# Kernel tuning notes

Measured on AMD Instinct MI355X. Metric: run time of the kernel, lower is better.

Reference implementation:

```python
import jax, jax.numpy as jnp
import numpy as np
import math

NUM_HEADS = 16
HEAD_SIZE = 64
QKT_MEAN = 0.0
QKT_STD = 0.05
APPLY_NOISE = True
NOISE_KEY = jax.random.key(42)


def quantize_activation_8bit(x):
    max_abs = jnp.maximum(jnp.max(jnp.abs(x)), 1e-08)
    scale = max_abs / 127.0
    return jnp.clip(jnp.round(x / scale), -127, 127) * scale


def quantize_weight_4bit(w):
    max_abs = jnp.maximum(jnp.max(jnp.abs(w)), 1e-08)
    scale = max_abs / 7.0
    return jnp.clip(jnp.round(w / scale), -7, 7) * scale


def setup_inputs() -> dict:
    key = jax.random.key(0)
    k1, k2, k3, k4 = jax.random.split(key, 4)
    B, S, D = 4, 1024, 1024
    hidden_states = jax.random.normal(k1, (B, S, D), dtype=jnp.float32)
    attention_mask = jnp.zeros((B, 1, 1, S), dtype=jnp.float32)
    # nn.Linear weights are [out_features, in_features]
    w_scale = 1.0 / math.sqrt(D)
    Wq = jax.random.normal(k2, (D, D), dtype=jnp.float32) * w_scale
    Wk = jax.random.normal(k3, (D, D), dtype=jnp.float32) * w_scale
    Wv = jax.random.normal(k4, (D, D), dtype=jnp.float32) * w_scale
    return {"hidden_states": hidden_states, "attention_mask": attention_mask,
            "Wq": Wq, "Wk": Wk, "Wv": Wv}


def _split_heads(x):
    B, S, _ = x.shape
    return x.reshape(B, S, NUM_HEADS, HEAD_SIZE).transpose(0, 2, 1, 3)  # [B,H,S,Dh]


def reference(hidden_states, attention_mask, Wq, Wk, Wv):
    h_q = quantize_activation_8bit(hidden_states)
    h_k = quantize_activation_8bit(hidden_states)
    Q = _split_heads(jnp.einsum('bsd,od->bso', h_q, quantize_weight_4bit(Wq)))
    K = _split_heads(jnp.einsum('bsd,od->bso', h_k, quantize_weight_4bit(Wk)))
    V = _split_heads(jnp.einsum('bsd,od->bso', hidden_states, quantize_weight_4bit(Wv)))
    qkt = jnp.einsum('bhqd,bhkd->bhqk', Q, K) / math.sqrt(HEAD_SIZE)
    if APPLY_NOISE and QKT_STD > 0:
        noise = jax.random.normal(NOISE_KEY, qkt.shape, dtype=qkt.dtype) * QKT_STD + QKT_MEAN
        qkt = qkt + noise
    qkt = qkt + attention_mask  # [B,1,1,S] broadcasts over [B,H,S,S]
    attn_weights = jax.nn.softmax(qkt, axis=-1)  # dropout is identity in eval
    ctx = jnp.einsum('bhqk,bhkd->bhqd', attn_weights, V)
    B, H, S, Dh = ctx.shape
    ctx = ctx.transpose(0, 2, 1, 3).reshape(B, S, H * Dh)
    return ctx
```

## Files before the change

kernel.cpp:

```cpp
#include <hip/hip_runtime.h>
#include <hip/hip_bf16.h>

typedef unsigned short u16;
typedef unsigned int u32;
typedef __bf16 bf16x8 __attribute__((ext_vector_type(8)));
typedef float f32x4 __attribute__((ext_vector_type(4)));

#define MFMA16(a, b, c) __builtin_amdgcn_mfma_f32_16x16x32_bf16((a), (b), (c), 0, 0, 0)

static __device__ __forceinline__ float bfbits2f(u32 b) {
    union { u32 u; float f; } c; c.u = b << 16; return c.f;
}
static __device__ __forceinline__ u32 f2bfbits(float f) {
    union { float f; u32 u; } c; c.f = f;
    return (c.u + 0x7FFFu + ((c.u >> 16) & 1u)) >> 16;
}
static __device__ __forceinline__ u32 f2bfbits_exact(float f) {
    union { float f; u32 u; } c; c.f = f;
    return c.u >> 16;
}
static __device__ __forceinline__ u32 pack_bf16x2(float lo, float hi) {
    float2 v; v.x = lo; v.y = hi;
    union { __hip_bfloat162 h; u32 u; } c;
    c.h = __float22bfloat162_rn(v);
    return c.u;
}

static __device__ __forceinline__ void noise_pu8(const u32* __restrict__ idx,
                                                 float* __restrict__ pu) {
    const u32 K1 = 42u, K2 = 0x1BD11BF0u;
    u32 x0[8], x1[8];
#pragma unroll
    for (int d = 0; d < 8; d++) { x0[d] = 0u; x1[d] = idx[d] + K1; }
#define TFR(R)                                            \
    _Pragma("unroll") for (int d = 0; d < 8; d++) {       \
        x0[d] += x1[d];                                   \
        x1[d] = __builtin_rotateleft32(x1[d], R) ^ x0[d]; \
    }
#define INJ(A, B)                                         \
    _Pragma("unroll") for (int d = 0; d < 8; d++) {       \
        x0[d] += (A); x1[d] += (B);                       \
    }
    TFR(13) TFR(15) TFR(26) TFR(6)  INJ(K1, K2 + 1u)
    TFR(17) TFR(29) TFR(16) TFR(24) INJ(K2, 2u)
    TFR(13) TFR(15) TFR(26) TFR(6)  INJ(0u, K1 + 3u)
    TFR(17) TFR(29) TFR(16) TFR(24) INJ(K1, K2 + 4u)
    TFR(13) TFR(15) TFR(26) TFR(6)  INJ(K2, 5u)
#undef TFR
#undef INJ
#pragma unroll
    for (int d = 0; d < 8; d++) {
        u32 bits = x0[d] ^ x1[d];
        float f = __uint_as_float((bits >> 9) | 0x3F800000u) - 1.0f;
        float u = fmaf(f, 2.0f, -0.99999994f);
        u = fmaxf(-0.99999994f, u);
        float t = fmaf(-u, u, 1.0f);
        float lg = __logf(t);
        float p;
        if (lg > -5.0f) {
            float z = fmaf(lg, -1.0f, -2.5f);
            p = 2.81022636e-08f;
            p = fmaf(p, z, 3.43273939e-07f);
            p = fmaf(p, z, -3.5233877e-06f);
            p = fmaf(p, z, -4.39150654e-06f);
            p = fmaf(p, z, 0.00021858087f);
            p = fmaf(p, z, -0.00125372503f);
            p = fmaf(p, z, -0.00417768164f);
            p = fmaf(p, z, 0.246640727f);
            p = fmaf(p, z, 1.50140941f);
        } else {
            float z = sqrtf(-lg) - 3.0f;
            p = -0.000200214257f;
            p = fmaf(p, z, 0.000100950558f);
            p = fmaf(p, z, 0.00134934322f);
            p = fmaf(p, z, -0.00367342844f);
            p = fmaf(p, z, 0.00573950773f);
            p = fmaf(p, z, -0.0076224613f);
            p = fmaf(p, z, 0.00943887047f);
            p = fmaf(p, z, 1.00167406f);
            p = fmaf(p, z, 2.83297682f);
        }
        pu[d] = p * u;
    }
}

__global__ __launch_bounds__(256) void absmax_k(const float* __restrict__ h,
                                                const float* __restrict__ wq,
                                                const float* __restrict__ wk,
                                                const float* __restrict__ wv,
                                                u32* __restrict__ slots) {
    int t = blockIdx.y;
    const float* src = (t == 0) ? h : (t == 1) ? wq : (t == 2) ? wk : wv;
    int n4 = ((t == 0) ? 4096 * 1024 : 1024 * 1024) / 4;
    u32 mx = 0;
    int tid = threadIdx.x;
    for (int i = blockIdx.x * blockDim.x + tid; i < n4; i += gridDim.x * blockDim.x) {
        uint4 v = ((const uint4*)src)[i];
        mx = max(mx, v.x & 0x7FFFFFFFu);
        mx = max(mx, v.y & 0x7FFFFFFFu);
        mx = max(mx, v.z & 0x7FFFFFFFu);
        mx = max(mx, v.w & 0x7FFFFFFFu);
    }
    __shared__ u32 red[256];
    red[tid] = mx;
    __syncthreads();
    for (int s = 128; s > 0; s >>= 1) {
        if (tid < s) red[tid] = max(red[tid], red[tid + s]);
        __syncthreads();
    }
    if (tid == 0) atomicMax(&slots[t], red[0]);
}

__global__ __launch_bounds__(256) void prequant_all(const float* __restrict__ hidden,
                                                    const float* __restrict__ wq,
                                                    const float* __restrict__ wk,
                                                    const float* __restrict__ wv,
                                                    u16* __restrict__ hq,
                                                    u16* __restrict__ hbf,
                                                    u16* __restrict__ wqi,
                                                    u16* __restrict__ wki,
                                                    u16* __restrict__ wvi,
                                                    const u32* __restrict__ slots) {
    int y = blockIdx.y;
    const float* src = (y == 0) ? hidden : (y == 1) ? wq : (y == 2) ? wk : wv;
    u16* dqi = (y == 0) ? hq : (y == 1) ? wqi : (y == 2) ? wki : wvi;
    u16* draw = (y == 0) ? hbf : nullptr;
    float qmax = (y == 0) ? 127.0f : 7.0f;
    int n8 = ((y == 0) ? 4096 * 1024 : 1024 * 1024) / 8;

    float amax = fmaxf(__uint_as_float(slots[y]), 1e-8f);
    float scale = amax / qmax;
    for (int i = blockIdx.x * blockDim.x + threadIdx.x; i < n8; i += gridDim.x * blockDim.x) {
        float4 a = ((const float4*)src)[2 * i];
        float4 b = ((const float4*)src)[2 * i + 1];
        float x[8] = {a.x, a.y, a.z, a.w, b.x, b.y, b.z, b.w};
        u16 qi[8], rw[8];
#pragma unroll
        for (int j = 0; j < 8; j++) {
            float q = fminf(fmaxf(rintf(x[j] / scale), -qmax), qmax);
            qi[j] = (u16)f2bfbits_exact(q);
            rw[j] = (u16)f2bfbits(x[j]);
        }
        *(uint4*)(dqi + 8 * (size_t)i) = *(const uint4*)qi;
        if (draw) *(uint4*)(draw + 8 * (size_t)i) = *(const uint4*)rw;
    }
}

__global__ __launch_bounds__(256) void qkv_gemm_all(const u16* __restrict__ hq,
                                                    const u16* __restrict__ hbf,
                                                    const u16* __restrict__ wqi,
                                                    const u16* __restrict__ wki,
                                                    const u16* __restrict__ wvi,
                                                    const u32* __restrict__ slots,
                                                    u16* __restrict__ Qb,
                                                    u16* __restrict__ Kb,
                                                    u16* __restrict__ Vtb) {
    __shared__ __align__(16) u16 As[64 * 40];
    __shared__ __align__(16) u16 Bs[64 * 40];
    int z = blockIdx.z;
    const u16* A  = (z < 2) ? hq : hbf;
    const u16* Bw = (z == 0) ? wqi : (z == 1) ? wki : wvi;
    u16* outp     = (z == 0) ? Qb : (z == 1) ? Kb : Vtb;
    int transOut = (z == 2);
    float s_a = fmaxf(__uint_as_float(slots[0]), 1e-8f) / 127.0f;
    float s_w = fmaxf(__uint_as_float(slots[z + 1]), 1e-8f) / 7.0f;
    float oscale = (z < 2) ? (s_a * s_w) : s_w;

    int tid = threadIdx.x;
    int srow = tid >> 2, scol = (tid & 3) * 8;
    int mbase = blockIdx.x * 64, nbase = blockIdx.y * 64;
    int lane = tid & 63, wv = tid >> 6;
    int quad = lane >> 4, l16 = lane & 15;

    f32x4 acc[4];
#pragma unroll
    for (int i = 0; i < 4; i++) acc[i] = (f32x4){0.f, 0.f, 0.f, 0.f};

    const u16* aptr = A + (size_t)(mbase + srow) * 1024 + scol;
    const u16* bptr = Bw + (size_t)(nbase + srow) * 1024 + scol;

    for (int k0 = 0; k0 < 1024; k0 += 32) {
        uint4 av = *(const uint4*)(aptr + k0);
        uint4 bv = *(const uint4*)(bptr + k0);
        __syncthreads();
        *(uint4*)(As + srow * 40 + scol) = av;
        *(uint4*)(Bs + srow * 40 + scol) = bv;
        __syncthreads();
        bf16x8 af = *(const bf16x8*)(As + (wv * 16 + l16) * 40 + quad * 8);
#pragma unroll
        for (int nt = 0; nt < 4; nt++) {
            bf16x8 bfr = *(const bf16x8*)(Bs + (nt * 16 + l16) * 40 + quad * 8);
            acc[nt] = MFMA16(af, bfr, acc[nt]);
        }
    }

#pragma unroll
    for (int nt = 0; nt < 4; nt++) {
#pragma unroll
        for (int r = 0; r < 4; r++) {
            float val = acc[nt][r] * oscale;
            int m = mbase + wv * 16 + quad * 4 + r;
            int o = nbase + nt * 16 + l16;
            int b = m >> 10, s = m & 1023;
            int hh = o >> 6, dh = o & 63;
            size_t off = transOut ? (((size_t)(b * 16 + hh) * 64 + dh) * 1024 + s)
                                  : (((size_t)(b * 16 + hh) * 1024 + s) * 64 + dh);
            outp[off] = (u16)f2bfbits(val);
        }
    }
}

__global__ __launch_bounds__(256, 2) void attn_kernel(const u16* __restrict__ Q,
                                                      const u16* __restrict__ K,
                                                      const u16* __restrict__ Vt,
                                                      const float* __restrict__ mask,
                                                      float* __restrict__ O0,
                                                      float* __restrict__ O1,
                                                      float* __restrict__ l0,
                                                      float* __restrict__ l1) {
    __shared__ __align__(16) u16 Plds[2][4][16][40];
    int qt = blockIdx.x, h = blockIdx.y;
    int b = blockIdx.z & 3, split = blockIdx.z >> 2;
    int bh = b * 16 + h;
    int tid = threadIdx.x, wv = tid >> 6, lane = tid & 63;
    int quad = lane >> 4, l16 = lane & 15;
    int q0 = qt * 64 + wv * 16;
    int ks0 = split * 512;

    float* Obuf = split ? O1 : O0;
    float* lbuf = split ? l1 : l0;

    const u16* Qb = Q + (size_t)bh * 1024 * 64;
    const u16* Kb = K + (size_t)bh * 1024 * 64;
    const u16* Vb = Vt + (size_t)bh * 64 * 1024;

    bf16x8 aq0 = *(const bf16x8*)(Qb + (q0 + l16) * 64 + quad * 8);
    bf16x8 aq1 = *(const bf16x8*)(Qb + (q0 + l16) * 64 + 32 + quad * 8);

    f32x4 oacc[4];
#pragma unroll
    for (int i = 0; i < 4; i++) oacc[i] = (f32x4){0.f, 0.f, 0.f, 0.f};
    float lsum[4] = {0.f, 0.f, 0.f, 0.f};

    u16* Pw0 = &Plds[0][wv][0][0];
    u16* Pw1 = &Plds[1][wv][0][0];
    u32 idxbase = ((u32)bh * 1024u + (u32)(q0 + quad * 4)) * 1024u;
    const float* maskb = mask + b * 1024;

    for (int ks = ks0; ks < ks0 + 512; ks += 32) {
        f32x4 s0 = (f32x4){0.f, 0.f, 0.f, 0.f};
        f32x4 s1 = (f32x4){0.f, 0.f, 0.f, 0.f};
        const u16* Kt = Kb + (size_t)ks * 64;
        bf16x8 bk0 = *(const bf16x8*)(Kt + l16 * 64 + quad * 8);
        bf16x8 bk1 = *(const bf16x8*)(Kt + l16 * 64 + 32 + quad * 8);
        bf16x8 bk2 = *(const bf16x8*)(Kt + (16 + l16) * 64 + quad * 8);
        bf16x8 bk3 = *(const bf16x8*)(Kt + (16 + l16) * 64 + 32 + quad * 8);
        s0 = MFMA16(aq0, bk0, s0);
        s0 = MFMA16(aq1, bk1, s0);
        s1 = MFMA16(aq0, bk2, s1);
        s1 = MFMA16(aq1, bk3, s1);

        int kg0 = ks + l16;
        float mk0 = maskb[kg0];
        float mk1 = maskb[kg0 + 16];

        u32 idxs[8];
        float pu[8];
#pragma unroll
        for (int r = 0; r < 4; r++) {
            u32 idx = idxbase + (u32)r * 1024u + (u32)kg0;
            idxs[2 * r] = idx;
            idxs[2 * r + 1] = idx + 16u;
        }
        noise_pu8(idxs, pu);

        u16* myP = ((ks >> 5) & 1) ? Pw1 : Pw0;
#pragma unroll
        for (int r = 0; r < 4; r++) {
            float sv0 = fmaf(pu[2 * r], 0.07071067811865475f, fmaf(s0[r], 0.125f, mk0));
            float sv1 = fmaf(pu[2 * r + 1], 0.07071067811865475f, fmaf(s1[r], 0.125f, mk1));
            u32 pk = pack_bf16x2(__expf(sv0), __expf(sv1));
            myP[(quad * 4 + r) * 40 + l16] = (u16)pk;
            myP[(quad * 4 + r) * 40 + 16 + l16] = (u16)(pk >> 16);
            lsum[r] += bfbits2f(pk & 0xFFFFu) + bfbits2f(pk >> 16);
        }

        asm volatile("" ::: "memory");
        bf16x8 pf = *(const bf16x8*)(myP + l16 * 40 + quad * 8);
        asm volatile("" ::: "memory");
        const u16* Vk = Vb + ks;
#pragma unroll
        for (int nt = 0; nt < 4; nt++) {
            bf16x8 vf = *(const bf16x8*)(Vk + (nt * 16 + l16) * 1024 + quad * 8);
            oacc[nt] = MFMA16(pf, vf, oacc[nt]);
        }
    }

    float lred[4];
#pragma unroll
    for (int r = 0; r < 4; r++) {
        float l = lsum[r];
        l += __shfl_xor(l, 1);
        l += __shfl_xor(l, 2);
        l += __shfl_xor(l, 4);
        l += __shfl_xor(l, 8);
        lred[r] = l;
    }
    if (l16 == 0) {
        int lbase = bh * 1024 + q0 + quad * 4;
#pragma unroll
        for (int r = 0; r < 4; r++) lbuf[lbase + r] = lred[r];
    }
#pragma unroll
    for (int nt = 0; nt < 4; nt++) {
#pragma unroll
        for (int r = 0; r < 4; r++) {
            int q = q0 + quad * 4 + r;
            int dh = nt * 16 + l16;
            Obuf[((size_t)(b * 1024 + q)) * 1024 + h * 64 + dh] = oacc[nt][r];
        }
    }
}

__global__ __launch_bounds__(256) void combine_k(float* __restrict__ outp,
                                                 const float* __restrict__ O1,
                                                 const float* __restrict__ l0,
                                                 const float* __restrict__ l1) {
    int gid = blockIdx.x * 256 + threadIdx.x;
    int e = gid << 2;
    int bq = e >> 10;
    int h = (e & 1023) >> 6;
    int b = bq >> 10, q = bq & 1023;
    int lidx = ((b * 16 + h) << 10) + q;
    float linv = 1.0f / (l0[lidx] + l1[lidx]);
    float4 a = ((const float4*)outp)[gid];
    float4 c = ((const float4*)O1)[gid];
    float4 o;
    o.x = (a.x + c.x) * linv;
    o.y = (a.y + c.y) * linv;
    o.z = (a.z + c.z) * linv;
    o.w = (a.w + c.w) * linv;
    ((float4*)outp)[gid] = o;
}

extern "C" void kernel_launch(void* const* d_in, const int* in_sizes, int n_in,
                              void* d_out, int out_size, void* d_ws, size_t ws_size,
                              hipStream_t stream) {
    (void)in_sizes; (void)n_in; (void)out_size; (void)ws_size;
    const float* hidden = (const float*)d_in[0];
    const float* maskp  = (const float*)d_in[1];
    const float* Wq     = (const float*)d_in[2];
    const float* Wk     = (const float*)d_in[3];
    const float* Wv     = (const float*)d_in[4];
    float* outp = (float*)d_out;

    char* ws = (char*)d_ws;
    u32* slots = (u32*)ws;
    u16* hq  = (u16*)(ws + 256);
    u16* hbf = hq + 4096 * 1024;
    u16* wqi = hbf + 4096 * 1024;
    u16* wki = wqi + 1024 * 1024;
    u16* wvi = wki + 1024 * 1024;
    u16* Qb  = wvi + 1024 * 1024;
    u16* Kb  = Qb + 4096 * 1024;
    u16* Vtb = Kb + 4096 * 1024;

    float* O1buf = (float*)hq;
    float* l0buf = (float*)wqi;
    float* l1buf = l0buf + 4 * 16 * 1024;

    hipMemsetAsync(slots, 0, 16, stream);
    absmax_k<<<dim3(128, 4), 256, 0, stream>>>(hidden, Wq, Wk, Wv, slots);
    prequant_all<<<dim3(64, 4), 256, 0, stream>>>(hidden, Wq, Wk, Wv,
                                                  hq, hbf, wqi, wki, wvi, slots);
    qkv_gemm_all<<<dim3(64, 16, 3), 256, 0, stream>>>(hq, hbf, wqi, wki, wvi, slots,
                                                      Qb, Kb, Vtb);
    attn_kernel<<<dim3(16, 16, 8), 256, 0, stream>>>(Qb, Kb, Vtb, maskp,
                                                     outp, O1buf, l0buf, l1buf);
    combine_k<<<dim3(4096), 256, 0, stream>>>(outp, O1buf, l0buf, l1buf);
}
```

Measured before the change: 389.2 us.

## Enlarge QKV GEMM tiles to 128x128, simplify noise erfinv, sum fp32 probabilities

The QKV projection GEMM moves from 64x64 to 128x128 block tiles, with each wave computing a 4x4 grid of MFMA tiles, so LDS-staged operands are reused more and fewer blocks are launched. The Gaussian noise generator drops the two-branch erfinv polynomial in favour of a single branch on log2 with a clamp. That removes divergence but changes the tail accuracy of the noise. The softmax denominator now accumulates the fp32 exponentials instead of the bf16-rounded values, saving conversions at the cost of a slight mismatch with the packed P.

New measurement: 350.4 us. 10.0% less time.

```diff
diff --git a/kernel.cpp b/kernel.cpp
--- a/kernel.cpp
+++ b/kernel.cpp
@@ -51,35 +51,21 @@
 #pragma unroll
     for (int d = 0; d < 8; d++) {
         u32 bits = x0[d] ^ x1[d];
-        float f = __uint_as_float((bits >> 9) | 0x3F800000u) - 1.0f;
-        float u = fmaf(f, 2.0f, -0.99999994f);
-        u = fmaxf(-0.99999994f, u);
+        float v2 = __uint_as_float((bits >> 9) | 0x40000000u);
+        float u = v2 - 3.0f;
         float t = fmaf(-u, u, 1.0f);
-        float lg = __logf(t);
-        float p;
-        if (lg > -5.0f) {
-            float z = fmaf(lg, -1.0f, -2.5f);
-            p = 2.81022636e-08f;
-            p = fmaf(p, z, 3.43273939e-07f);
-            p = fmaf(p, z, -3.5233877e-06f);
-            p = fmaf(p, z, -4.39150654e-06f);
-            p = fmaf(p, z, 0.00021858087f);
-            p = fmaf(p, z, -0.00125372503f);
-            p = fmaf(p, z, -0.00417768164f);
-            p = fmaf(p, z, 0.246640727f);
-            p = fmaf(p, z, 1.50140941f);
-        } else {
-            float z = sqrtf(-lg) - 3.0f;
-            p = -0.000200214257f;
-            p = fmaf(p, z, 0.000100950558f);
-            p = fmaf(p, z, 0.00134934322f);
-            p = fmaf(p, z, -0.00367342844f);
-            p = fmaf(p, z, 0.00573950773f);
-            p = fmaf(p, z, -0.0076224613f);
-            p = fmaf(p, z, 0.00943887047f);
-            p = fmaf(p, z, 1.00167406f);
-            p = fmaf(p, z, 2.83297682f);
-        }
+        float L2 = __log2f(t);
+        L2 = fmaxf(L2, -7.2134752f);
+        float z = fmaf(L2, -0.69314718f, -2.5f);
+        float p = 2.81022636e-08f;
+        p = fmaf(p, z, 3.43273939e-07f);
+        p = fmaf(p, z, -3.5233877e-06f);
+        p = fmaf(p, z, -4.39150654e-06f);
+        p = fmaf(p, z, 0.00021858087f);
+        p = fmaf(p, z, -0.00125372503f);
+        p = fmaf(p, z, -0.00417768164f);
+        p = fmaf(p, z, 0.246640727f);
+        p = fmaf(p, z, 1.50140941f);
         pu[d] = p * u;
     }
 }
@@ -146,17 +132,17 @@
     }
 }
 
-__global__ __launch_bounds__(256) void qkv_gemm_all(const u16* __restrict__ hq,
-                                                    const u16* __restrict__ hbf,
-                                                    const u16* __restrict__ wqi,
-                                                    const u16* __restrict__ wki,
-                                                    const u16* __restrict__ wvi,
-                                                    const u32* __restrict__ slots,
-                                                    u16* __restrict__ Qb,
-                                                    u16* __restrict__ Kb,
-                                                    u16* __restrict__ Vtb) {
-    __shared__ __align__(16) u16 As[64 * 40];
-    __shared__ __align__(16) u16 Bs[64 * 40];
+__global__ __launch_bounds__(256, 2) void qkv_gemm_all(const u16* __restrict__ hq,
+                                                       const u16* __restrict__ hbf,
+                                                       const u16* __restrict__ wqi,
+                                                       const u16* __restrict__ wki,
+                                                       const u16* __restrict__ wvi,
+                                                       const u32* __restrict__ slots,
+                                                       u16* __restrict__ Qb,
+                                                       u16* __restrict__ Kb,
+                                                       u16* __restrict__ Vtb) {
+    __shared__ __align__(16) u16 As[128 * 40];
+    __shared__ __align__(16) u16 Bs[128 * 40];
     int z = blockIdx.z;
     const u16* A  = (z < 2) ? hq : hbf;
     const u16* Bw = (z == 0) ? wqi : (z == 1) ? wki : wvi;
@@ -168,46 +154,62 @@
 
     int tid = threadIdx.x;
     int srow = tid >> 2, scol = (tid & 3) * 8;
-    int mbase = blockIdx.x * 64, nbase = blockIdx.y * 64;
-    int lane = tid & 63, wv = tid >> 6;
+    int mbase = blockIdx.x * 128, nbase = blockIdx.y * 128;
+    int lane = tid & 63, w = tid >> 6;
+    int wv_m = w & 1, wv_n = w >> 1;
     int quad = lane >> 4, l16 = lane & 15;
 
-    f32x4 acc[4];
-#pragma unroll
-    for (int i = 0; i < 4; i++) acc[i] = (f32x4){0.f, 0.f, 0.f, 0.f};
-
-    const u16* aptr = A + (size_t)(mbase + srow) * 1024 + scol;
-    const u16* bptr = Bw + (size_t)(nbase + srow) * 1024 + scol;
+    f32x4 acc[4][4];
+#pragma unroll
+    for (int i = 0; i < 4; i++)
+#pragma unroll
+        for (int j = 0; j < 4; j++) acc[i][j] = (f32x4){0.f, 0.f, 0.f, 0.f};
+
+    const u16* aptr0 = A + (size_t)(mbase + srow) * 1024 + scol;
+    const u16* aptr1 = A + (size_t)(mbase + 64 + srow) * 1024 + scol;
+    const u16* bptr0 = Bw + (size_t)(nbase + srow) * 1024 + scol;
+    const u16* bptr1 = Bw + (size_t)(nbase + 64 + srow) * 1024 + scol;
 
     for (int k0 = 0; k0 < 1024; k0 += 32) {
-        uint4 av = *(const uint4*)(aptr + k0);
-        uint4 bv = *(const uint4*)(bptr + k0);
+        uint4 a0 = *(const uint4*)(aptr0 + k0);
+        uint4 a1 = *(const uint4*)(aptr1 + k0);
+        uint4 b0 = *(const uint4*)(bptr0 + k0);
+        uint4 b1 = *(const uint4*)(bptr1 + k0);
         __syncthreads();
-        *(uint4*)(As + srow * 40 + scol) = av;
-        *(uint4*)(Bs + srow * 40 + scol) = bv;
+        *(uint4*)(As + srow * 40 + scol) = a0;
+        *(uint4*)(As + (64 + srow) * 40 + scol) = a1;
+        *(uint4*)(Bs + srow * 40 + scol) = b0;
+        *(uint4*)(Bs + (64 + srow) * 40 + scol) = b1;
         __syncthreads();
-        bf16x8 af = *(const bf16x8*)(As + (wv * 16 + l16) * 40 + quad * 8);
-#pragma unroll
-        for (int nt = 0; nt < 4; nt++) {
-            bf16x8 bfr = *(const bf16x8*)(Bs + (nt * 16 + l16) * 40 + quad * 8);
-            acc[nt] = MFMA16(af, bfr, acc[nt]);
-        }
-    }
-
-#pragma unroll
-    for (int nt = 0; nt < 4; nt++) {
-#pragma unroll
-        for (int r = 0; r < 4; r++) {
-            float val = acc[nt][r] * oscale;
-            int m = mbase + wv * 16 + quad * 4 + r;
-            int o = nbase + nt * 16 + l16;
-            int b = m >> 10, s = m & 1023;
-            int hh = o >> 6, dh = o & 63;
-            size_t off = transOut ? (((size_t)(b * 16 + hh) * 64 + dh) * 1024 + s)
-                                  : (((size_t)(b * 16 + hh) * 1024 + s) * 64 + dh);
-            outp[off] = (u16)f2bfbits(val);
-        }
-    }
+        bf16x8 af[4], bfr[4];
+#pragma unroll
+        for (int mt = 0; mt < 4; mt++)
+            af[mt] = *(const bf16x8*)(As + (wv_m * 64 + mt * 16 + l16) * 40 + quad * 8);
+#pragma unroll
+        for (int nt = 0; nt < 4; nt++)
+            bfr[nt] = *(const bf16x8*)(Bs + (wv_n * 64 + nt * 16 + l16) * 40 + quad * 8);
+#pragma unroll
+        for (int mt = 0; mt < 4; mt++)
+#pragma unroll
+            for (int nt = 0; nt < 4; nt++)
+                acc[mt][nt] = MFMA16(af[mt], bfr[nt], acc[mt][nt]);
+    }
+
+#pragma unroll
+    for (int mt = 0; mt < 4; mt++)
+#pragma unroll
+        for (int nt = 0; nt < 4; nt++)
+#pragma unroll
+            for (int r = 0; r < 4; r++) {
+                float val = acc[mt][nt][r] * oscale;
+                int m = mbase + wv_m * 64 + mt * 16 + quad * 4 + r;
+                int o = nbase + wv_n * 64 + nt * 16 + l16;
+                int b = m >> 10, s = m & 1023;
+                int hh = o >> 6, dh = o & 63;
+                size_t off = transOut ? (((size_t)(b * 16 + hh) * 64 + dh) * 1024 + s)
+                                      : (((size_t)(b * 16 + hh) * 1024 + s) * 64 + dh);
+                outp[off] = (u16)f2bfbits(val);
+            }
 }
 
 __global__ __launch_bounds__(256, 2) void attn_kernel(const u16* __restrict__ Q,
@@ -279,10 +281,12 @@
         for (int r = 0; r < 4; r++) {
             float sv0 = fmaf(pu[2 * r], 0.07071067811865475f, fmaf(s0[r], 0.125f, mk0));
             float sv1 = fmaf(pu[2 * r + 1], 0.07071067811865475f, fmaf(s1[r], 0.125f, mk1));
-            u32 pk = pack_bf16x2(__expf(sv0), __expf(sv1));
+            float e0 = __expf(sv0);
+            float e1 = __expf(sv1);
+            u32 pk = pack_bf16x2(e0, e1);
             myP[(quad * 4 + r) * 40 + l16] = (u16)pk;
             myP[(quad * 4 + r) * 40 + 16 + l16] = (u16)(pk >> 16);
-            lsum[r] += bfbits2f(pk & 0xFFFFu) + bfbits2f(pk >> 16);
+            lsum[r] += e0 + e1;
         }
 
         asm volatile("" ::: "memory");
@@ -373,8 +377,8 @@
     absmax_k<<<dim3(128, 4), 256, 0, stream>>>(hidden, Wq, Wk, Wv, slots);
     prequant_all<<<dim3(64, 4), 256, 0, stream>>>(hidden, Wq, Wk, Wv,
                                                   hq, hbf, wqi, wki, wvi, slots);
-    qkv_gemm_all<<<dim3(64, 16, 3), 256, 0, stream>>>(hq, hbf, wqi, wki, wvi, slots,
-                                                      Qb, Kb, Vtb);
+    qkv_gemm_all<<<dim3(32, 8, 3), 256, 0, stream>>>(hq, hbf, wqi, wki, wvi, slots,
+                                                     Qb, Kb, Vtb);
     attn_kernel<<<dim3(16, 16, 8), 256, 0, stream>>>(Qb, Kb, Vtb, maskp,
                                                      outp, O1buf, l0buf, l1buf);
     combine_k<<<dim3(4096), 256, 0, stream>>>(outp, O1buf, l0buf, l1buf);
```
